# Performance work log

Measured on AMD Instinct MI355X. Metric: run time of the kernel, lower is better.

Reference implementation:

```python
import jax, jax.numpy as jnp
import numpy as np

NEG_SLOPE = 0.01  # nn.LeakyReLU default negative_slope


def setup_inputs() -> dict:
    key = jax.random.key(0)
    k1, k2 = jax.random.split(key)
    B, N, D = 32, 128, 128
    embeddings = jax.random.normal(k1, (B, N, D), dtype=jnp.float32)
    # nn.Linear(em_dim, 1): weight [1, D] -> stored as [D], bias [1]
    att_w = jax.random.normal(k2, (D,), dtype=jnp.float32) * (1.0 / np.sqrt(D))
    att_b = jnp.zeros((1,), dtype=jnp.float32)
    return {"embeddings": embeddings, "att_w": att_w, "att_b": att_b}


def reference(embeddings, att_w, att_b):
    # query[b,i,j,d] = e[b,i,d]; key[b,i,j,d] = e[b,j,d]
    # value = query * key : [B, N, N, D]
    value = embeddings[:, :, None, :] * embeddings[:, None, :, :]
    # Linear(D -> 1): scores[b,i,j] = sum_d value[b,i,j,d] * w[d] + b
    scores = jnp.einsum('bijd,d->bij', value, att_w) + att_b[0]
    scores = jnp.where(scores >= 0, scores, NEG_SLOPE * scores)  # LeakyReLU
    # dropout is identity in eval mode
    alphas = jax.nn.softmax(scores, axis=-1)[..., None]  # [B, N, N, 1]
    return alphas, value
```

## Files before the change

### kernel.cpp

```cpp
#include <hip/hip_runtime.h>
#include <cstddef>

#define B_ 32
#define N_ 128
#define D_ 128
#define NEG_SLOPE 0.01f

typedef float v4f __attribute__((ext_vector_type(4)));

__global__ void __launch_bounds__(256)
fused_value_attn_kernel(const float* __restrict__ e,
                        const float* __restrict__ w,
                        const float* __restrict__ bias,
                        float* __restrict__ alphas,
                        float* __restrict__ value) {
    const int bi = blockIdx.x;
    const int b  = bi >> 7;
    const int t  = threadIdx.x;
    const int d4 = t & 31;
    const int jg = t >> 5;

    __shared__ float sc[N_];
    __shared__ float red[N_];

    const v4f* __restrict__ e4 = reinterpret_cast<const v4f*>(e);
    const v4f w4  = reinterpret_cast<const v4f*>(w)[d4];
    const v4f ei4 = e4[(size_t)bi * 32 + d4];
    const float bias0 = bias[0];

    v4f* __restrict__ vout = reinterpret_cast<v4f*>(
        value + (size_t)bi * N_ * D_);

#pragma unroll 4
    for (int jj = 0; jj < 16; ++jj) {
        const int j = (jj << 3) + jg;
        const v4f ej4 = e4[((size_t)((b << 7) | j)) * 32 + d4];
        const v4f v4 = ei4 * ej4;

        __builtin_nontemporal_store(v4, &vout[(j << 5) + d4]);

        const v4f pw = v4 * w4;
        float p = pw.x + pw.y + pw.z + pw.w;
        p += __shfl_xor(p, 1);
        p += __shfl_xor(p, 2);
        p += __shfl_xor(p, 4);
        p += __shfl_xor(p, 8);
        p += __shfl_xor(p, 16);
        if (d4 == 0) sc[j] = p;
    }
    __syncthreads();

    float s = 0.f, ex = 0.f;
    if (t < N_) {
        s = sc[t] + bias0;
        s = (s >= 0.f) ? s : NEG_SLOPE * s;
        red[t] = s;
    }
    __syncthreads();
#pragma unroll
    for (int off = 64; off > 0; off >>= 1) {
        if (t < off) red[t] = fmaxf(red[t], red[t + off]);
        __syncthreads();
    }
    const float m = red[0];
    __syncthreads();
    if (t < N_) { ex = expf(s - m); red[t] = ex; }
    __syncthreads();
#pragma unroll
    for (int off = 64; off > 0; off >>= 1) {
        if (t < off) red[t] += red[t + off];
        __syncthreads();
    }
    if (t < N_) alphas[(size_t)bi * N_ + t] = ex / red[0];
}

extern "C" void kernel_launch(void* const* d_in, const int* in_sizes, int n_in,
                              void* d_out, int out_size, void* d_ws, size_t ws_size,
                              hipStream_t stream) {
    const float* e    = (const float*)d_in[0];
    const float* w    = (const float*)d_in[1];
    const float* bias = (const float*)d_in[2];

    float* out    = (float*)d_out;
    float* alphas = out;
    float* value  = out + (size_t)B_ * N_ * N_;

    fused_value_attn_kernel<<<B_ * N_, 256, 0, stream>>>(e, w, bias, alphas, value);
}
```

Baseline: 58.22 us.

## Process four query rows per block and use wave-shuffle softmax

Each block now computes four rows i, reusing each loaded e_j across them and precomputing e_i*w so the score dot product needs one multiply per element. The softmax reduction moves from a shared-memory tree with many barriers to per-wave shuffle reductions, one wave per row. The grid shrinks by four. The value stores no longer use the nontemporal hint, which may change cache and write behaviour on this store-bound kernel.

```diff
diff --git a/kernel.cpp b/kernel.cpp
--- a/kernel.cpp
+++ b/kernel.cpp
@@ -4,6 +4,7 @@
 #define B_ 32
 #define N_ 128
 #define D_ 128
+#define IT 4
 #define NEG_SLOPE 0.01f
 
 typedef float v4f __attribute__((ext_vector_type(4)));
@@ -14,64 +15,65 @@
                         const float* __restrict__ bias,
                         float* __restrict__ alphas,
                         float* __restrict__ value) {
-    const int bi = blockIdx.x;
-    const int b  = bi >> 7;
-    const int t  = threadIdx.x;
-    const int d4 = t & 31;
-    const int jg = t >> 5;
+    const int blk = blockIdx.x;
+    const int b   = blk >> 5;
+    const int i0  = (blk & 31) << 2;
+    const int t   = threadIdx.x;
+    const int d4  = t & 31;
+    const int jg  = t >> 5;
 
-    __shared__ float sc[N_];
-    __shared__ float red[N_];
+    __shared__ float sc[IT][N_];
 
     const v4f* __restrict__ e4 = reinterpret_cast<const v4f*>(e);
-    const v4f w4  = reinterpret_cast<const v4f*>(w)[d4];
-    const v4f ei4 = e4[(size_t)bi * 32 + d4];
-    const float bias0 = bias[0];
+    const v4f w4 = reinterpret_cast<const v4f*>(w)[d4];
 
-    v4f* __restrict__ vout = reinterpret_cast<v4f*>(
-        value + (size_t)bi * N_ * D_);
+    v4f ei4[IT], h4[IT];
+    v4f* vptr[IT];
+#pragma unroll
+    for (int q = 0; q < IT; ++q) {
+        const int bi = (b << 7) | (i0 + q);
+        ei4[q] = e4[(size_t)bi * 32 + d4];
+        h4[q]  = ei4[q] * w4;
+        vptr[q] = reinterpret_cast<v4f*>(value + (size_t)bi * N_ * D_);
+    }
 
 #pragma unroll 4
     for (int jj = 0; jj < 16; ++jj) {
         const int j = (jj << 3) + jg;
         const v4f ej4 = e4[((size_t)((b << 7) | j)) * 32 + d4];
-        const v4f v4 = ei4 * ej4;
-
-        __builtin_nontemporal_store(v4, &vout[(j << 5) + d4]);
-
-        const v4f pw = v4 * w4;
-        float p = pw.x + pw.y + pw.z + pw.w;
-        p += __shfl_xor(p, 1);
-        p += __shfl_xor(p, 2);
-        p += __shfl_xor(p, 4);
-        p += __shfl_xor(p, 8);
-        p += __shfl_xor(p, 16);
-        if (d4 == 0) sc[j] = p;
+#pragma unroll
+        for (int q = 0; q < IT; ++q) {
+            vptr[q][(j << 5) + d4] = ei4[q] * ej4;
+            const v4f pw = h4[q] * ej4;
+            float p = pw.x + pw.y + pw.z + pw.w;
+            p += __shfl_xor(p, 1);
+            p += __shfl_xor(p, 2);
+            p += __shfl_xor(p, 4);
+            p += __shfl_xor(p, 8);
+            p += __shfl_xor(p, 16);
+            if (d4 == 0) sc[q][j] = p;
+        }
     }
     __syncthreads();
 
-    float s = 0.f, ex = 0.f;
-    if (t < N_) {
-        s = sc[t] + bias0;
-        s = (s >= 0.f) ? s : NEG_SLOPE * s;
-        red[t] = s;
-    }
-    __syncthreads();
+    const int wv = t >> 6;
+    const int l  = t & 63;
+    const float bias0 = bias[0];
+    float s0 = sc[wv][l]      + bias0;
+    float s1 = sc[wv][l + 64] + bias0;
+    s0 = (s0 >= 0.f) ? s0 : NEG_SLOPE * s0;
+    s1 = (s1 >= 0.f) ? s1 : NEG_SLOPE * s1;
+    float m = fmaxf(s0, s1);
 #pragma unroll
-    for (int off = 64; off > 0; off >>= 1) {
-        if (t < off) red[t] = fmaxf(red[t], red[t + off]);
-        __syncthreads();
-    }
-    const float m = red[0];
-    __syncthreads();
-    if (t < N_) { ex = expf(s - m); red[t] = ex; }
-    __syncthreads();
+    for (int off = 32; off > 0; off >>= 1) m = fmaxf(m, __shfl_xor(m, off));
+    const float e0 = expf(s0 - m), e1 = expf(s1 - m);
+    float sum = e0 + e1;
 #pragma unroll
-    for (int off = 64; off > 0; off >>= 1) {
-        if (t < off) red[t] += red[t + off];
-        __syncthreads();
-    }
-    if (t < N_) alphas[(size_t)bi * N_ + t] = ex / red[0];
+    for (int off = 32; off > 0; off >>= 1) sum += __shfl_xor(sum, off);
+    const float inv = 1.f / sum;
+    float* arow = alphas + ((size_t)((b << 7) | (i0 + wv))) * N_;
+    arow[l]      = e0 * inv;
+    arow[l + 64] = e1 * inv;
 }
 
 extern "C" void kernel_launch(void* const* d_in, const int* in_sizes, int n_in,
@@ -85,5 +87,5 @@
     float* alphas = out;
     float* value  = out + (size_t)B_ * N_ * N_;
 
-    fused_value_attn_kernel<<<B_ * N_, 256, 0, stream>>>(e, w, bias, alphas, value);
+    fused_value_attn_kernel<<<(B_ * N_) / IT, 256, 0, stream>>>(e, w, bias, alphas, value);
 }
```

Result: faster. 49.86 us (-14.4%).
